# Performance work log

Hardware: AMD Instinct MI355X
Metric: run time of the kernel (lower is better)

Reference implementation:

```python
import jax, jax.numpy as jnp
import numpy as np

B, T, O = 32, 2048, 18            # batch, triples per graph, hardcoded object count
DIN1, H, DOUT = 1500, 512, 512    # net1 input dim is hardcoded 1500 in the source

def _kaiming(key, fan_in, fan_out):
    return jax.random.normal(key, (fan_in, fan_out), jnp.float32) * np.sqrt(2.0 / fan_in)

def setup_inputs() -> dict:
    key = jax.random.key(0)
    ks = jax.random.split(key, 8)
    trip = jax.random.normal(ks[0], (B, T, DIN1), jnp.float32)
    index = jax.random.randint(ks[1], (B, T, 2), 0, O)
    rel_lens = jax.random.randint(ks[2], (B,), 0, T)
    # net1: 1500 -> H -> 2H+Dout (ReLU after every layer incl. last)
    w1a = _kaiming(ks[3], DIN1, H); b1a = jnp.zeros((H,), jnp.float32)
    w1b = _kaiming(ks[4], H, 2 * H + DOUT); b1b = jnp.zeros((2 * H + DOUT,), jnp.float32)
    # net2: H -> H -> Dout (ReLU after every layer incl. last)
    w2a = _kaiming(ks[5], H, H); b2a = jnp.zeros((H,), jnp.float32)
    w2b = _kaiming(ks[6], H, DOUT); b2b = jnp.zeros((DOUT,), jnp.float32)
    return dict(trip=trip, index=index, rel_lens=rel_lens,
                w1a=w1a, b1a=b1a, w1b=w1b, b1b=b1b,
                w2a=w2a, b2a=b2a, w2b=w2b, b2b=b2b)

def reference(trip, index, rel_lens, w1a, b1a, w1b, b1b, w2a, b2a, w2b, b2b):
    # net1 MLP over all triples: [B,T,1500] -> [B,T,2H+Dout]
    h = jax.nn.relu(trip @ w1a + b1a)
    new_t = jax.nn.relu(h @ w1b + b1b)
    s_vecs = new_t[..., :H]              # [B,T,H] subject
    p_vecs = new_t[..., H:H + DOUT]      # [B,T,Dout] predicate (returned as-is)
    o_vecs = new_t[..., H + DOUT:]       # [B,T,H] object
    # mask out triples beyond rel_lens[i]
    mask = (jnp.arange(T)[None, :] < rel_lens[:, None]).astype(new_t.dtype)  # [B,T]
    oh_s = jax.nn.one_hot(index[..., 0], O, dtype=new_t.dtype) * mask[..., None]  # [B,T,O]
    oh_o = jax.nn.one_hot(index[..., 1], O, dtype=new_t.dtype) * mask[..., None]
    # per-batch scatter_add pooling into the O=18 object slots
    contrib = (jnp.einsum('bto,bth->boh', oh_s, s_vecs)
               + jnp.einsum('bto,bth->boh', oh_o, o_vecs))  # [B,O,H]
    # original code never resets pooled_obj_vecs inside the batch loop ->
    # accumulation is CUMULATIVE over batch items
    pooled = jnp.cumsum(contrib, axis=0)  # [B,O,H]
    # net2 MLP on each cumulative pool
    h2 = jax.nn.relu(pooled @ w2a + b2a)
    new_obj = jax.nn.relu(h2 @ w2b + b2b)  # [B,O,Dout]
    return new_obj, p_vecs
```

## Files before the change

### kernel.cpp

```cpp
#include <hip/hip_runtime.h>
#include <hip/hip_bf16.h>

#define NBATCH 32
#define NTIME  2048
#define NOBJ   18
#define KIN    1500
#define NH     512
#define NTOT   1536
#define NM     65536

typedef __attribute__((ext_vector_type(4))) float f32x4;
typedef __attribute__((ext_vector_type(8))) short s16x8;
typedef __attribute__((ext_vector_type(4))) short s16x4;

static __device__ __forceinline__ short f2bf(float f) {
  union { float f; unsigned u; } v; v.f = f;
  unsigned r = v.u + 0x7fffu + ((v.u >> 16) & 1u);
  return (short)(r >> 16);
}

static __device__ __forceinline__ void gload_lds16(const short* g, short* l) {
  __builtin_amdgcn_global_load_lds(
      (const __attribute__((address_space(1))) unsigned int*)(g),
      (__attribute__((address_space(3))) unsigned int*)(l), 16, 0, 0);
}

#define FENCE() asm volatile("" ::: "memory")
#define BAR()   do { FENCE(); __builtin_amdgcn_s_barrier(); FENCE(); } while (0)
#define LGKM0() asm volatile("s_waitcnt lgkmcnt(0)" ::: "memory")

__global__ void k_prep(const float* __restrict__ src, short* __restrict__ dst,
                       int K, int Nsrc, int nkt, int total) {
  int i = blockIdx.x * 256 + threadIdx.x;
  if (i >= total) return;
  int chunk = i >> 14, off = i & 16383;
  int row = off >> 6, kcp = off & 63;
  int kc = kcp ^ ((row & 7) << 3);
  int cb = chunk / nkt, kt = chunk - cb * nkt;
  int n = cb * 256 + row, k = kt * 64 + kc;
  dst[i] = (k < K) ? f2bf(src[(size_t)k * Nsrc + n]) : (short)0;
}

__global__ void k_zero(float* __restrict__ p, int n) {
  int i = blockIdx.x * 256 + threadIdx.x;
  if (i < n) p[i] = 0.f;
}

__launch_bounds__(512, 2)
__global__ void k_gemm1(const float* __restrict__ A, const short* __restrict__ Bc,
                        const float* __restrict__ bias, short* __restrict__ Hc) {
  __shared__ short lA[2][256 * 64];
  __shared__ short lB[2][256 * 64];
  const int g = blockIdx.x;
  const int lid = (g & 7) * 64 + (g >> 3);
  const int rb = lid >> 1, cb = lid & 1;
  const int m0 = rb * 256, n0 = cb * 256;
  const int tid = threadIdx.x;
  const int lane = tid & 63, w = tid >> 6;
  const int wr = w >> 2, wc = w & 3;
  const int rlane = lane & 15, ksel = (lane >> 4) * 8;
  const int swz = (rlane & 7) << 3;
  const int kx0 = ksel ^ swz, kx1 = (32 | ksel) ^ swz;
  const int arow = tid >> 4;
  const int akq  = (tid & 15) * 4;
  const short* bchunk = Bc + (size_t)(cb * 24) * 16384;

  f32x4 acc[8][4] = {};
  float4 av[4];
  s16x8 af[4][2];
  s16x8 bf0[2][2], bf1[2][2];

  auto issueA_h = [&](int kt, int h) {
    const int kbase = kt * 64;
    const bool fullq = (kt < 23) | (akq <= 24);
#pragma unroll
    for (int i = 0; i < 4; ++i) {
      const float* p = A + (size_t)(m0 + arow + (h * 4 + i) * 32) * KIN + kbase + akq;
      av[i] = fullq ? *(const float4*)p : make_float4(0.f, 0.f, 0.f, 0.f);
    }
  };
  auto writeA_h = [&](int nb, int h) {
#pragma unroll
    for (int i = 0; i < 4; ++i) {
      int r = arow + (h * 4 + i) * 32;
      s16x4 h4;
      h4[0] = f2bf(av[i].x); h4[1] = f2bf(av[i].y);
      h4[2] = f2bf(av[i].z); h4[3] = f2bf(av[i].w);
      *(s16x4*)&lA[nb][r * 64 + (akq ^ ((r & 7) << 3))] = h4;
    }
  };
  auto issueB = [&](int nb, int kt, int h) {
    const short* src = bchunk + (size_t)kt * 16384 + h * 8192 + tid * 8;
#pragma unroll
    for (int j = 0; j < 2; ++j)
      gload_lds16(src + j * 4096, &lB[nb][h * 8192 + tid * 8 + j * 4096]);
  };
  auto readA = [&](int cu, int rh) {
#pragma unroll
    for (int mm = 0; mm < 4; ++mm) {
      int ro = (rh * 128 + wr * 64 + mm * 16 + rlane) * 64;
      af[mm][0] = *(const s16x8*)&lA[cu][ro + kx0];
      af[mm][1] = *(const s16x8*)&lA[cu][ro + kx1];
    }
  };
  auto readB = [&](int cu, int ch, s16x8 (&dst)[2][2]) {
#pragma unroll
    for (int qn = 0; qn < 2; ++qn) {
      int ro = (ch * 128 + wc * 32 + qn * 16 + rlane) * 64;
      dst[qn][0] = *(const s16x8*)&lB[cu][ro + kx0];
      dst[qn][1] = *(const s16x8*)&lB[cu][ro + kx1];
    }
  };
  auto mfma_quad = [&](int rh, int ch, s16x8 (&bfr)[2][2]) {
    __builtin_amdgcn_s_setprio(1);
#pragma unroll
    for (int j = 0; j < 2; ++j)
#pragma unroll
      for (int mm = 0; mm < 4; ++mm)
#pragma unroll
        for (int qn = 0; qn < 2; ++qn)
          acc[rh * 4 + mm][ch * 2 + qn] = __builtin_amdgcn_mfma_f32_16x16x32_bf16(
              af[mm][j], bfr[qn][j], acc[rh * 4 + mm][ch * 2 + qn], 0, 0, 0);
    __builtin_amdgcn_s_setprio(0);
  };

  issueA_h(0, 0);
  issueB(0, 0, 0);
  writeA_h(0, 0);
  issueA_h(0, 1);
  issueB(0, 0, 1);
  writeA_h(0, 1);
  issueA_h(1, 0);
  LGKM0();
  BAR();

#pragma unroll 1
  for (int kt = 0; kt < 24; ++kt) {
    const int cu = kt & 1, nb = cu ^ 1;
    const bool hn = kt < 23, hn2 = kt < 22;
    readA(cu, 0); readB(cu, 0, bf0);
    if (hn) issueB(nb, kt + 1, 0);
    if (hn) { asm volatile("s_waitcnt vmcnt(6)" ::: "memory"); }
    else    { asm volatile("s_waitcnt vmcnt(0)" ::: "memory"); }
    BAR(); LGKM0();
    mfma_quad(0, 0, bf0);
    BAR();
    readB(cu, 1, bf1);
    if (hn) { writeA_h(nb, 0); issueA_h(kt + 1, 1); }
    BAR(); LGKM0();
    mfma_quad(0, 1, bf1);
    BAR();
    readA(cu, 1);
    if (hn) issueB(nb, kt + 1, 1);
    BAR(); LGKM0();
    mfma_quad(1, 1, bf1);
    BAR();
    if (hn) writeA_h(nb, 1);
    if (hn2) issueA_h(kt + 2, 0);
    LGKM0();
    BAR();
    mfma_quad(1, 0, bf0);
    BAR();
  }

#pragma unroll
  for (int n = 0; n < 4; ++n) {
    int c = n0 + (n >> 1) * 128 + wc * 32 + (n & 1) * 16 + rlane;
    float bv = bias[c];
#pragma unroll
    for (int m = 0; m < 8; ++m) {
      int rbase = m0 + (m >> 2) * 128 + wr * 64 + (m & 3) * 16 + ((lane >> 4) << 2);
#pragma unroll
      for (int q = 0; q < 4; ++q) {
        int r = rbase + q;
        float v = acc[m][n][q] + bv;
        v = v > 0.f ? v : 0.f;
        Hc[(size_t)(((r >> 8) * 8 + (c >> 6)) * 16384) + (r & 255) * 64 +
           ((c & 63) ^ ((r & 7) << 3))] = f2bf(v);
      }
    }
  }
}

__launch_bounds__(512, 2)
__global__ void k_gemm2(const short* __restrict__ Ac, const short* __restrict__ Bc,
                        const float* __restrict__ bias, const int* __restrict__ index,
                        const int* __restrict__ rel_lens,
                        float* __restrict__ contrib, float* __restrict__ out) {
  __shared__ short lA[2][256 * 64];
  __shared__ short lB[2][256 * 64];
  const int g = blockIdx.x;
  const int lid = (g & 7) * 192 + (g >> 3);
  const int rb = lid / 6, cb = lid - rb * 6;
  const int m0 = rb * 256;
  const int tid = threadIdx.x;
  const int lane = tid & 63, w = tid >> 6;
  const int wr = w >> 2, wc = w & 3;
  const int rlane = lane & 15, ksel = (lane >> 4) * 8;
  const int swz = (rlane & 7) << 3;
  const int kx0 = ksel ^ swz, kx1 = (32 | ksel) ^ swz;
  const short* achunk = Ac + (size_t)(rb * 8) * 16384;
  const short* bchunk = Bc + (size_t)(cb * 8) * 16384;

  f32x4 acc[8][4] = {};
  s16x8 af[4][2], bf0[2][2], bf1[2][2];

  auto issueA = [&](int nb, int kt, int h) {
    const short* src = achunk + (size_t)kt * 16384 + h * 8192 + tid * 8;
#pragma unroll
    for (int j = 0; j < 2; ++j)
      gload_lds16(src + j * 4096, &lA[nb][h * 8192 + tid * 8 + j * 4096]);
  };
  auto issueB = [&](int nb, int kt, int h) {
    const short* src = bchunk + (size_t)kt * 16384 + h * 8192 + tid * 8;
#pragma unroll
    for (int j = 0; j < 2; ++j)
      gload_lds16(src + j * 4096, &lB[nb][h * 8192 + tid * 8 + j * 4096]);
  };
  auto readA = [&](int cu, int rh) {
#pragma unroll
    for (int mm = 0; mm < 4; ++mm) {
      int ro = (rh * 128 + wr * 64 + mm * 16 + rlane) * 64;
      af[mm][0] = *(const s16x8*)&lA[cu][ro + kx0];
      af[mm][1] = *(const s16x8*)&lA[cu][ro + kx1];
    }
  };
  auto readB = [&](int cu, int ch, s16x8 (&dst)[2][2]) {
#pragma unroll
    for (int qn = 0; qn < 2; ++qn) {
      int ro = (ch * 128 + wc * 32 + qn * 16 + rlane) * 64;
      dst[qn][0] = *(const s16x8*)&lB[cu][ro + kx0];
      dst[qn][1] = *(const s16x8*)&lB[cu][ro + kx1];
    }
  };
  auto mfma_quad = [&](int rh, int ch, s16x8 (&bfr)[2][2]) {
    __builtin_amdgcn_s_setprio(1);
#pragma unroll
    for (int j = 0; j < 2; ++j)
#pragma unroll
      for (int mm = 0; mm < 4; ++mm)
#pragma unroll
        for (int qn = 0; qn < 2; ++qn)
          acc[rh * 4 + mm][ch * 2 + qn] = __builtin_amdgcn_mfma_f32_16x16x32_bf16(
              af[mm][j], bfr[qn][j], acc[rh * 4 + mm][ch * 2 + qn], 0, 0, 0);
    __builtin_amdgcn_s_setprio(0);
  };

  issueA(0, 0, 0);
  issueB(0, 0, 0);
  issueB(0, 0, 1);
  issueA(0, 0, 1);
  asm volatile("s_waitcnt vmcnt(4)" ::: "memory");
  BAR();

#pragma unroll 1
  for (int kt = 0; kt < 8; ++kt) {
    const int cu = kt & 1, nb = cu ^ 1;
    const bool hn = kt < 7;
    readA(cu, 0); readB(cu, 0, bf0);
    if (hn) issueA(nb, kt + 1, 0);
    if (hn) { asm volatile("s_waitcnt vmcnt(4)" ::: "memory"); }
    else    { asm volatile("s_waitcnt vmcnt(2)" ::: "memory"); }
    BAR(); LGKM0();
    mfma_quad(0, 0, bf0);
    BAR();
    readB(cu, 1, bf1);
    if (hn) issueB(nb, kt + 1, 0);
    if (hn) { asm volatile("s_waitcnt vmcnt(4)" ::: "memory"); }
    else    { asm volatile("s_waitcnt vmcnt(0)" ::: "memory"); }
    BAR(); LGKM0();
    mfma_quad(0, 1, bf1);
    BAR();
    readA(cu, 1);
    if (hn) issueB(nb, kt + 1, 1);
    BAR(); LGKM0();
    mfma_quad(1, 1, bf1);
    BAR();
    if (hn) issueA(nb, kt + 1, 1);
    if (hn) { asm volatile("s_waitcnt vmcnt(4)" ::: "memory"); }
    BAR();
    mfma_quad(1, 0, bf0);
    BAR();
  }

  const int region = cb >> 1;
  float bv[4]; int cg[4];
#pragma unroll
  for (int n = 0; n < 4; ++n) {
    cg[n] = cb * 256 + (n >> 1) * 128 + wc * 32 + (n & 1) * 16 + rlane;
    bv[n] = bias[cg[n]];
  }

  if (region == 1) {
    float* po = out + (size_t)NBATCH * NOBJ * NH;
#pragma unroll
    for (int m = 0; m < 8; ++m) {
      int rbase = m0 + (m >> 2) * 128 + wr * 64 + (m & 3) * 16 + ((lane >> 4) << 2);
#pragma unroll
      for (int q = 0; q < 4; ++q) {
#pragma unroll
        for (int n = 0; n < 4; ++n) {
          float v = acc[m][n][q] + bv[n];
          v = v > 0.f ? v : 0.f;
          po[(size_t)(rbase + q) * NH + (cg[n] & 511)] = v;
        }
      }
    }
  } else {
    const int sel = region >> 1;
    const int b = m0 >> 11;
    const int rel = rel_lens[b];
#pragma unroll
    for (int m = 0; m < 8; ++m) {
      int rbase = m0 + (m >> 2) * 128 + wr * 64 + (m & 3) * 16 + ((lane >> 4) << 2);
#pragma unroll
      for (int q = 0; q < 4; ++q) {
        int r = rbase + q;
        if ((r & 2047) < rel) {
          int idx = index[2 * r + sel];
          float* dst = contrib + ((b * NOBJ + idx) << 9);
#pragma unroll
          for (int n = 0; n < 4; ++n) {
            float v = acc[m][n][q] + bv[n];
            v = v > 0.f ? v : 0.f;
            atomicAdd(dst + (cg[n] & 511), v);
          }
        }
      }
    }
  }
}

__global__ void k_cumsum(const float* __restrict__ contrib, float* __restrict__ pooled) {
  int i = blockIdx.x * 256 + threadIdx.x;
  if (i >= NOBJ * NH) return;
  float a = 0.f;
#pragma unroll
  for (int b = 0; b < NBATCH; ++b) {
    a += contrib[b * (NOBJ * NH) + i];
    pooled[b * (NOBJ * NH) + i] = a;
  }
}

__global__ void k_mlp2(const float* __restrict__ pooled,
                       const float* __restrict__ w2a, const float* __restrict__ b2a,
                       const float* __restrict__ w2b, const float* __restrict__ b2b,
                       float* __restrict__ out) {
  __shared__ float pr[NH];
  __shared__ float hr[NH];
  int row = blockIdx.x;
  int tid = threadIdx.x;
  pr[tid]       = pooled[(size_t)row * NH + tid];
  pr[tid + 256] = pooled[(size_t)row * NH + tid + 256];
  __syncthreads();
  float s0 = 0.f, s1 = 0.f;
  for (int k = 0; k < NH; ++k) {
    float p = pr[k];
    s0 += p * w2a[k * NH + tid];
    s1 += p * w2a[k * NH + tid + 256];
  }
  s0 += b2a[tid]; s1 += b2a[tid + 256];
  hr[tid]       = s0 > 0.f ? s0 : 0.f;
  hr[tid + 256] = s1 > 0.f ? s1 : 0.f;
  __syncthreads();
  s0 = 0.f; s1 = 0.f;
  for (int k = 0; k < NH; ++k) {
    float h = hr[k];
    s0 += h * w2b[k * NH + tid];
    s1 += h * w2b[k * NH + tid + 256];
  }
  s0 += b2b[tid]; s1 += b2b[tid + 256];
  out[(size_t)row * NH + tid]       = s0 > 0.f ? s0 : 0.f;
  out[(size_t)row * NH + tid + 256] = s1 > 0.f ? s1 : 0.f;
}

extern "C" void kernel_launch(void* const* d_in, const int* in_sizes, int n_in,
                              void* d_out, int out_size, void* d_ws, size_t ws_size,
                              hipStream_t stream) {
  const float* trip     = (const float*)d_in[0];
  const int*   index    = (const int*)d_in[1];
  const int*   rel_lens = (const int*)d_in[2];
  const float* w1a      = (const float*)d_in[3];
  const float* b1a      = (const float*)d_in[4];
  const float* w1b      = (const float*)d_in[5];
  const float* b1b      = (const float*)d_in[6];
  const float* w2a      = (const float*)d_in[7];
  const float* b2a      = (const float*)d_in[8];
  const float* w2b      = (const float*)d_in[9];
  const float* b2b      = (const float*)d_in[10];
  float* out = (float*)d_out;

  char* ws = (char*)d_ws;
  short* wt1a    = (short*)(ws);
  short* wt1b    = (short*)(ws + 1572864);
  short* hbuf    = (short*)(ws + 3145728);
  float* contrib = (float*)(ws + 70254592);
  float* pooled  = contrib + NBATCH * NOBJ * NH;

  k_prep<<<3072, 256, 0, stream>>>(w1a, wt1a, KIN, NH, 24, NH * 1536);
  k_prep<<<3072, 256, 0, stream>>>(w1b, wt1b, NH, NTOT, 8, NTOT * NH);
  k_zero<<<1152, 256, 0, stream>>>(contrib, NBATCH * NOBJ * NH);
  k_gemm1<<<512, 512, 0, stream>>>(trip, wt1a, b1a, hbuf);
  k_gemm2<<<1536, 512, 0, stream>>>(hbuf, wt1b, b1b, index, rel_lens, contrib, out);
  k_cumsum<<<36, 256, 0, stream>>>(contrib, pooled);
  k_mlp2<<<576, 256, 0, stream>>>(pooled, w2a, b2a, w2b, b2b, out);
}
```

Before: 487.6 us.

## Collapse per-phase barriers into one sync per K-tile in both GEMMs

Both GEMM kernels drop the four barrier/waitcnt pairs per K iteration and keep a single waitcnt plus barrier at the end of each tile. Next-tile loads for the whole tile are issued early, and the A staging uses two register sets so both halves are prefetched two tiles ahead. This is meant to cut barrier stalls and let MFMA overlap global loads. The cost is higher register pressure, and correctness now relies on the double-buffered LDS never being overwritten while another wave still reads it.

```diff
diff --git a/kernel.cpp b/kernel.cpp
--- a/kernel.cpp
+++ b/kernel.cpp
@@ -66,11 +66,11 @@
   const short* bchunk = Bc + (size_t)(cb * 24) * 16384;
 
   f32x4 acc[8][4] = {};
-  float4 av[4];
+  float4 av0[4], av1[4];
   s16x8 af[4][2];
   s16x8 bf0[2][2], bf1[2][2];
 
-  auto issueA_h = [&](int kt, int h) {
+  auto issueA_h = [&](int kt, int h, float4 (&av)[4]) {
     const int kbase = kt * 64;
     const bool fullq = (kt < 23) | (akq <= 24);
 #pragma unroll
@@ -79,7 +79,7 @@
       av[i] = fullq ? *(const float4*)p : make_float4(0.f, 0.f, 0.f, 0.f);
     }
   };
-  auto writeA_h = [&](int nb, int h) {
+  auto writeA_h = [&](int nb, int h, float4 (&av)[4]) {
 #pragma unroll
     for (int i = 0; i < 4; ++i) {
       int r = arow + (h * 4 + i) * 32;
@@ -89,11 +89,11 @@
       *(s16x4*)&lA[nb][r * 64 + (akq ^ ((r & 7) << 3))] = h4;
     }
   };
-  auto issueB = [&](int nb, int kt, int h) {
-    const short* src = bchunk + (size_t)kt * 16384 + h * 8192 + tid * 8;
-#pragma unroll
-    for (int j = 0; j < 2; ++j)
-      gload_lds16(src + j * 4096, &lB[nb][h * 8192 + tid * 8 + j * 4096]);
+  auto issueB_full = [&](int nb, int kt) {
+    const short* src = bchunk + (size_t)kt * 16384 + tid * 8;
+#pragma unroll
+    for (int j = 0; j < 4; ++j)
+      gload_lds16(src + j * 4096, &lB[nb][tid * 8 + j * 4096]);
   };
   auto readA = [&](int cu, int rh) {
 #pragma unroll
@@ -124,43 +124,38 @@
     __builtin_amdgcn_s_setprio(0);
   };
 
-  issueA_h(0, 0);
-  issueB(0, 0, 0);
-  writeA_h(0, 0);
-  issueA_h(0, 1);
-  issueB(0, 0, 1);
-  writeA_h(0, 1);
-  issueA_h(1, 0);
+  issueA_h(0, 0, av0);
+  issueA_h(0, 1, av1);
+  issueB_full(0, 0);
+  writeA_h(0, 0, av0);
+  writeA_h(0, 1, av1);
+  issueA_h(1, 0, av0);
+  issueA_h(1, 1, av1);
+  asm volatile("s_waitcnt vmcnt(8)" ::: "memory");
   LGKM0();
   BAR();
 
 #pragma unroll 1
   for (int kt = 0; kt < 24; ++kt) {
     const int cu = kt & 1, nb = cu ^ 1;
-    const bool hn = kt < 23, hn2 = kt < 22;
     readA(cu, 0); readB(cu, 0, bf0);
-    if (hn) issueB(nb, kt + 1, 0);
-    if (hn) { asm volatile("s_waitcnt vmcnt(6)" ::: "memory"); }
-    else    { asm volatile("s_waitcnt vmcnt(0)" ::: "memory"); }
-    BAR(); LGKM0();
+    if (kt < 23) issueB_full(nb, kt + 1);
     mfma_quad(0, 0, bf0);
-    BAR();
     readB(cu, 1, bf1);
-    if (hn) { writeA_h(nb, 0); issueA_h(kt + 1, 1); }
-    BAR(); LGKM0();
+    if (kt < 23) writeA_h(nb, 0, av0);
     mfma_quad(0, 1, bf1);
-    BAR();
     readA(cu, 1);
-    if (hn) issueB(nb, kt + 1, 1);
-    BAR(); LGKM0();
+    if (kt < 22) issueA_h(kt + 2, 0, av0);
     mfma_quad(1, 1, bf1);
-    BAR();
-    if (hn) writeA_h(nb, 1);
-    if (hn2) issueA_h(kt + 2, 0);
-    LGKM0();
-    BAR();
+    if (kt < 23) writeA_h(nb, 1, av1);
+    if (kt < 22) issueA_h(kt + 2, 1, av1);
     mfma_quad(1, 0, bf0);
-    BAR();
+    if (kt < 23) {
+      if (kt < 22) { asm volatile("s_waitcnt vmcnt(8)" ::: "memory"); }
+      else         { asm volatile("s_waitcnt vmcnt(0)" ::: "memory"); }
+      LGKM0();
+      BAR();
+    }
   }
 
 #pragma unroll
@@ -205,17 +200,17 @@
   f32x4 acc[8][4] = {};
   s16x8 af[4][2], bf0[2][2], bf1[2][2];
 
-  auto issueA = [&](int nb, int kt, int h) {
-    const short* src = achunk + (size_t)kt * 16384 + h * 8192 + tid * 8;
-#pragma unroll
-    for (int j = 0; j < 2; ++j)
-      gload_lds16(src + j * 4096, &lA[nb][h * 8192 + tid * 8 + j * 4096]);
-  };
-  auto issueB = [&](int nb, int kt, int h) {
-    const short* src = bchunk + (size_t)kt * 16384 + h * 8192 + tid * 8;
-#pragma unroll
-    for (int j = 0; j < 2; ++j)
-      gload_lds16(src + j * 4096, &lB[nb][h * 8192 + tid * 8 + j * 4096]);
+  auto issueA_full = [&](int nb, int kt) {
+    const short* src = achunk + (size_t)kt * 16384 + tid * 8;
+#pragma unroll
+    for (int j = 0; j < 4; ++j)
+      gload_lds16(src + j * 4096, &lA[nb][tid * 8 + j * 4096]);
+  };
+  auto issueB_full = [&](int nb, int kt) {
+    const short* src = bchunk + (size_t)kt * 16384 + tid * 8;
+#pragma unroll
+    for (int j = 0; j < 4; ++j)
+      gload_lds16(src + j * 4096, &lB[nb][tid * 8 + j * 4096]);
   };
   auto readA = [&](int cu, int rh) {
 #pragma unroll
@@ -246,41 +241,26 @@
     __builtin_amdgcn_s_setprio(0);
   };
 
-  issueA(0, 0, 0);
-  issueB(0, 0, 0);
-  issueB(0, 0, 1);
-  issueA(0, 0, 1);
-  asm volatile("s_waitcnt vmcnt(4)" ::: "memory");
+  issueA_full(0, 0);
+  issueB_full(0, 0);
+  asm volatile("s_waitcnt vmcnt(0)" ::: "memory");
   BAR();
 
 #pragma unroll 1
   for (int kt = 0; kt < 8; ++kt) {
     const int cu = kt & 1, nb = cu ^ 1;
-    const bool hn = kt < 7;
     readA(cu, 0); readB(cu, 0, bf0);
-    if (hn) issueA(nb, kt + 1, 0);
-    if (hn) { asm volatile("s_waitcnt vmcnt(4)" ::: "memory"); }
-    else    { asm volatile("s_waitcnt vmcnt(2)" ::: "memory"); }
-    BAR(); LGKM0();
+    if (kt < 7) { issueA_full(nb, kt + 1); issueB_full(nb, kt + 1); }
     mfma_quad(0, 0, bf0);
-    BAR();
     readB(cu, 1, bf1);
-    if (hn) issueB(nb, kt + 1, 0);
-    if (hn) { asm volatile("s_waitcnt vmcnt(4)" ::: "memory"); }
-    else    { asm volatile("s_waitcnt vmcnt(0)" ::: "memory"); }
-    BAR(); LGKM0();
     mfma_quad(0, 1, bf1);
-    BAR();
     readA(cu, 1);
-    if (hn) issueB(nb, kt + 1, 1);
-    BAR(); LGKM0();
     mfma_quad(1, 1, bf1);
-    BAR();
-    if (hn) issueA(nb, kt + 1, 1);
-    if (hn) { asm volatile("s_waitcnt vmcnt(4)" ::: "memory"); }
-    BAR();
     mfma_quad(1, 0, bf0);
-    BAR();
+    if (kt < 7) {
+      asm volatile("s_waitcnt vmcnt(0)" ::: "memory");
+      BAR();
+    }
   }
 
   const int region = cb >> 1;
```

Measured after the change: 501.3 us. +2.8%, slower.
